# Optimization experiments

Hardware: AMD Instinct MI355X
Metric: run time of the kernel (lower is better)

## Reference

```python
import jax, jax.numpy as jnp
import numpy as np

B, N, D = 4, 4096, 128
R, K, O = 4, 16, 128


def setup_inputs() -> dict:
    key = jax.random.key(0)
    k1, k2, k3, k4 = jax.random.split(key, 4)
    node_features = jax.random.normal(k1, (B, N, D), dtype=jnp.float32)
    # index 0 selects the zero-pad row; valid node i is index i+1
    neighbor_indices = jax.random.randint(k2, (B, R, N, K), 0, N + 1, dtype=jnp.int32)
    relation_kernels = jax.random.normal(k3, (R, D, O), dtype=jnp.float32) * (1.0 / np.sqrt(D))
    self_kernel = jax.random.normal(k4, (D, O), dtype=jnp.float32) * (1.0 / np.sqrt(D))
    bias = jnp.zeros((O,), dtype=jnp.float32)
    return {
        "node_features": node_features,
        "neighbor_indices": neighbor_indices,
        "relation_kernels": relation_kernels,
        "self_kernel": self_kernel,
        "bias": bias,
    }


def reference(node_features, neighbor_indices, relation_kernels, self_kernel, bias):
    b, n, d = node_features.shape
    # prepend zero row so index 0 acts as padding (matches tf.concat zero_pad)
    padded = jnp.concatenate(
        [jnp.zeros((b, 1, d), node_features.dtype), node_features], axis=1
    )  # [B, N+1, D]
    # batched gather (tf.gather batch_dims=1): [B, R, N, K, D]
    neighbor_features = jax.vmap(lambda p, i: p[i])(padded, neighbor_indices)
    aggregated = neighbor_features.mean(axis=3)  # [B, R, N, D]
    # per-relation matmul then sum over relations
    total_msg = jnp.einsum("brnd,rdo->bno", aggregated, relation_kernels)
    self_msg = jnp.einsum("bnd,do->bno", node_features, self_kernel)
    out = total_msg + self_msg + bias
    return jax.nn.relu(out)  # dropout is identity at inference (rate=0.0)
```

## Files before the change

kernel.cpp:

```cpp
#include <hip/hip_runtime.h>
#include <cstddef>

namespace {
constexpr int B_ = 4, N_ = 4096, D_ = 128, R_ = 4, K_ = 16, O_ = 128;
constexpr int NP1 = N_ + 1;
constexpr int TN = 16;
constexpr int THREADS = 512;
constexpr int KK = (R_ + 1) * D_;
constexpr int PITCH_A = KK + 8;
}

typedef __bf16 bf16x8 __attribute__((ext_vector_type(8)));
typedef __bf16 bf16x4 __attribute__((ext_vector_type(4)));
typedef float  f32x4v __attribute__((ext_vector_type(4)));
typedef float  f32x2v __attribute__((ext_vector_type(2)));
using u32 = unsigned int;

__global__ __launch_bounds__(256)
void prep_all(const float* __restrict__ nf, const float* __restrict__ relk,
              const float* __restrict__ selfk,
              __bf16* __restrict__ ptab, unsigned char* __restrict__ ptab8,
              __bf16* __restrict__ wt) {
    int t = blockIdx.x * 256 + threadIdx.x;
    const int total_tab = B_ * NP1 * (D_ / 4);
    if (t < total_tab) {
        const int b   = t / (NP1 * 32);
        const int rem = t % (NP1 * 32);
        const int row = rem >> 5;
        const int q   = rem & 31;
        bf16x4 res;
        if (row == 0) {
            res[0] = (__bf16)0.f; res[1] = (__bf16)0.f;
            res[2] = (__bf16)0.f; res[3] = (__bf16)0.f;
        } else {
            const float4 v = *(const float4*)(nf + ((size_t)b * N_ + (row - 1)) * D_ + q * 4);
            res[0] = (__bf16)v.x; res[1] = (__bf16)v.y;
            res[2] = (__bf16)v.z; res[3] = (__bf16)v.w;
        }
        *(bf16x4*)(ptab + ((size_t)b * NP1 + row) * D_ + q * 4) = res;
        return;
    }
    t -= total_tab;
    if (t < total_tab) {
        const int b   = t / (NP1 * 32);
        const int rem = t % (NP1 * 32);
        const int row = rem >> 5;
        const int q   = rem & 31;
        u32 v8 = 0u;
        if (row != 0) {
            const float4 v = *(const float4*)(nf + ((size_t)b * N_ + (row - 1)) * D_ + q * 4);
            v8 = (u32)__builtin_amdgcn_cvt_pk_fp8_f32(v.x, v.y, 0, false);
            v8 = (u32)__builtin_amdgcn_cvt_pk_fp8_f32(v.z, v.w, (int)v8, true);
        }
        *(u32*)(ptab8 + ((size_t)b * NP1 + row) * D_ + q * 4) = v8;
        return;
    }
    t -= total_tab;
    if (t < O_ * (KK / 4)) {
        const int o   = t / (KK / 4);
        const int kk  = (t % (KK / 4)) * 4;
        bf16x4 res;
        #pragma unroll
        for (int i = 0; i < 4; ++i) {
            const int kki = kk + i;
            const float w = (kki < R_ * D_) ? relk[(size_t)kki * O_ + o]
                                            : selfk[(size_t)(kki - R_ * D_) * O_ + o];
            res[i] = (__bf16)w;
        }
        *(bf16x4*)(wt + (size_t)o * KK + kk) = res;
    }
}

__global__ __launch_bounds__(THREADS, 4)
void gcn_fused(const __bf16* __restrict__ ptab,
               const unsigned char* __restrict__ ptab8,
               const int*    __restrict__ nbr,
               const __bf16* __restrict__ wt,
               const float*  __restrict__ bias,
               float*        __restrict__ out)
{
    __shared__ __bf16 agg[TN][PITCH_A];

    const int hw   = blockIdx.x;
    const int xcd  = hw & 7;
    const int b    = xcd >> 1;
    const int tile = (xcd & 1) + ((hw >> 3) << 1);
    const int n0   = tile * TN;

    const int tid = threadIdx.x;
    const int wv  = tid >> 6;
    const int l   = tid & 63;

    {
        const int r    = wv & 3;
        const int nb   = (wv >> 2) * 8;
        const int nloc = l >> 3;
        const int cch  = l & 7;
        const int ioff = __builtin_amdgcn_readfirstlane(
            (((b * R_ + r) * N_) + n0 + nb) * K_);
        const int* __restrict__ ib = nbr + ioff;
        const unsigned char* __restrict__ tb8 = ptab8 + (size_t)b * NP1 * D_;

        f32x2v acc0 = {0.f,0.f}, acc1 = {0.f,0.f}, acc2 = {0.f,0.f}, acc3 = {0.f,0.f};
        f32x2v acc4 = {0.f,0.f}, acc5 = {0.f,0.f}, acc6 = {0.f,0.f}, acc7 = {0.f,0.f};

        #pragma unroll
        for (int k4 = 0; k4 < 4; ++k4) {
            const int4 iq = *(const int4*)(ib + nloc * K_ + k4 * 4);
            #define GCN_ROW(IDX)                                                   \
            {                                                                      \
                const uint4 u = *(const uint4*)(tb8 + (size_t)(IDX) * D_ + cch*16);\
                acc0 += __builtin_amdgcn_cvt_pk_f32_fp8(u.x, false);               \
                acc1 += __builtin_amdgcn_cvt_pk_f32_fp8(u.x, true);                \
                acc2 += __builtin_amdgcn_cvt_pk_f32_fp8(u.y, false);               \
                acc3 += __builtin_amdgcn_cvt_pk_f32_fp8(u.y, true);                \
                acc4 += __builtin_amdgcn_cvt_pk_f32_fp8(u.z, false);               \
                acc5 += __builtin_amdgcn_cvt_pk_f32_fp8(u.z, true);                \
                acc6 += __builtin_amdgcn_cvt_pk_f32_fp8(u.w, false);               \
                acc7 += __builtin_amdgcn_cvt_pk_f32_fp8(u.w, true);                \
            }
            GCN_ROW(iq.x) GCN_ROW(iq.y) GCN_ROW(iq.z) GCN_ROW(iq.w)
            #undef GCN_ROW
        }

        constexpr float s = 1.0f / (float)K_;
        bf16x8 r0, r1;
        r0[0] = (__bf16)(acc0.x * s); r0[1] = (__bf16)(acc0.y * s);
        r0[2] = (__bf16)(acc1.x * s); r0[3] = (__bf16)(acc1.y * s);
        r0[4] = (__bf16)(acc2.x * s); r0[5] = (__bf16)(acc2.y * s);
        r0[6] = (__bf16)(acc3.x * s); r0[7] = (__bf16)(acc3.y * s);
        r1[0] = (__bf16)(acc4.x * s); r1[1] = (__bf16)(acc4.y * s);
        r1[2] = (__bf16)(acc5.x * s); r1[3] = (__bf16)(acc5.y * s);
        r1[4] = (__bf16)(acc6.x * s); r1[5] = (__bf16)(acc6.y * s);
        r1[6] = (__bf16)(acc7.x * s); r1[7] = (__bf16)(acc7.y * s);
        __bf16* dst = &agg[nb + nloc][r * D_ + cch * 16];
        *(bf16x8*)(dst)     = r0;
        *(bf16x8*)(dst + 8) = r1;

        #pragma unroll
        for (int j = 0; j < 2; ++j) {
            const int n = wv * 2 + j;
            const u32 u = *((const u32*)(ptab + ((size_t)b * NP1 + n0 + n + 1) * D_) + l);
            *((u32*)&agg[n][R_ * D_] + l) = u;
        }
    }
    __syncthreads();

    const int lr = l & 15;
    const int lk = l >> 4;
    const int ct = wv;

    const __bf16* __restrict__ wr = wt + (size_t)(ct * 16 + lr) * KK + lk * 8;
    const __bf16* arow = &agg[lr][lk * 8];

    f32x4v acc = {0.f, 0.f, 0.f, 0.f};
    #pragma unroll 5
    for (int k0 = 0; k0 < KK; k0 += 32) {
        const bf16x8 a  = *(const bf16x8*)(arow + k0);
        const bf16x8 bf = *(const bf16x8*)(wr + k0);
        acc = __builtin_amdgcn_mfma_f32_16x16x32_bf16(a, bf, acc, 0, 0, 0);
    }

    const float bv = bias[ct * 16 + lr];
    #pragma unroll
    for (int j = 0; j < 4; ++j) {
        const int row = lk * 4 + j;
        out[((size_t)b * N_ + n0 + row) * O_ + ct * 16 + lr] = fmaxf(acc[j] + bv, 0.f);
    }
}

extern "C" void kernel_launch(void* const* d_in, const int* in_sizes, int n_in,
                              void* d_out, int out_size, void* d_ws, size_t ws_size,
                              hipStream_t stream) {
    const float* nf    = (const float*)d_in[0];
    const int*   nbr   = (const int*)  d_in[1];
    const float* relk  = (const float*)d_in[2];
    const float* selfk = (const float*)d_in[3];
    const float* bias  = (const float*)d_in[4];
    float* outp = (float*)d_out;

    __bf16* ptab = (__bf16*)d_ws;
    __bf16* wtp  = ptab + (size_t)B_ * NP1 * D_;
    unsigned char* ptab8 = (unsigned char*)(wtp + (size_t)O_ * KK);

    {
        const int total = 2 * B_ * NP1 * (D_ / 4) + O_ * (KK / 4);
        prep_all<<<(total + 255) / 256, 256, 0, stream>>>(nf, relk, selfk,
                                                          ptab, ptab8, wtp);
    }

    dim3 grid(B_ * (N_ / TN));
    gcn_fused<<<grid, THREADS, 0, stream>>>(ptab, ptab8, nbr, wtp, bias, outp);
}
```

Baseline: 37.17 us.

## Double node tile per block, reuse weight fragments across two MFMA row tiles

Raises the node tile from 16 to 32 per block so each weight fragment loaded from global memory feeds two MFMAs, halving weight traffic per output row and the number of blocks. The self-feature part of the GEMM now reads bf16 rows straight from global memory instead of staging them in shared memory, which shrinks the LDS tile. Each gather thread now handles two nodes with all index loads issued up front. The grid is halved (512 blocks), which lowers parallelism, and per-thread register pressure goes up.

```diff
diff --git a/kernel.cpp b/kernel.cpp
--- a/kernel.cpp
+++ b/kernel.cpp
@@ -4,10 +4,11 @@
 namespace {
 constexpr int B_ = 4, N_ = 4096, D_ = 128, R_ = 4, K_ = 16, O_ = 128;
 constexpr int NP1 = N_ + 1;
-constexpr int TN = 16;
+constexpr int TN = 32;
 constexpr int THREADS = 512;
 constexpr int KK = (R_ + 1) * D_;
-constexpr int PITCH_A = KK + 8;
+constexpr int KR = R_ * D_;
+constexpr int PITCH_A = KR + 8;
 }
 
 typedef __bf16 bf16x8 __attribute__((ext_vector_type(8)));
@@ -63,8 +64,8 @@
         #pragma unroll
         for (int i = 0; i < 4; ++i) {
             const int kki = kk + i;
-            const float w = (kki < R_ * D_) ? relk[(size_t)kki * O_ + o]
-                                            : selfk[(size_t)(kki - R_ * D_) * O_ + o];
+            const float w = (kki < KR) ? relk[(size_t)kki * O_ + o]
+                                       : selfk[(size_t)(kki - KR) * O_ + o];
             res[i] = (__bf16)w;
         }
         *(bf16x4*)(wt + (size_t)o * KK + kk) = res;
@@ -93,56 +94,73 @@
 
     {
         const int r    = wv & 3;
-        const int nb   = (wv >> 2) * 8;
+        const int ob   = (wv >> 2) * 8;
         const int nloc = l >> 3;
         const int cch  = l & 7;
         const int ioff = __builtin_amdgcn_readfirstlane(
-            (((b * R_ + r) * N_) + n0 + nb) * K_);
+            (((b * R_ + r) * N_) + n0) * K_);
         const int* __restrict__ ib = nbr + ioff;
         const unsigned char* __restrict__ tb8 = ptab8 + (size_t)b * NP1 * D_;
 
-        f32x2v acc0 = {0.f,0.f}, acc1 = {0.f,0.f}, acc2 = {0.f,0.f}, acc3 = {0.f,0.f};
-        f32x2v acc4 = {0.f,0.f}, acc5 = {0.f,0.f}, acc6 = {0.f,0.f}, acc7 = {0.f,0.f};
-
-        #pragma unroll
-        for (int k4 = 0; k4 < 4; ++k4) {
-            const int4 iq = *(const int4*)(ib + nloc * K_ + k4 * 4);
-            #define GCN_ROW(IDX)                                                   \
-            {                                                                      \
-                const uint4 u = *(const uint4*)(tb8 + (size_t)(IDX) * D_ + cch*16);\
-                acc0 += __builtin_amdgcn_cvt_pk_f32_fp8(u.x, false);               \
-                acc1 += __builtin_amdgcn_cvt_pk_f32_fp8(u.x, true);                \
-                acc2 += __builtin_amdgcn_cvt_pk_f32_fp8(u.y, false);               \
-                acc3 += __builtin_amdgcn_cvt_pk_f32_fp8(u.y, true);                \
-                acc4 += __builtin_amdgcn_cvt_pk_f32_fp8(u.z, false);               \
-                acc5 += __builtin_amdgcn_cvt_pk_f32_fp8(u.z, true);                \
-                acc6 += __builtin_amdgcn_cvt_pk_f32_fp8(u.w, false);               \
-                acc7 += __builtin_amdgcn_cvt_pk_f32_fp8(u.w, true);                \
-            }
-            GCN_ROW(iq.x) GCN_ROW(iq.y) GCN_ROW(iq.z) GCN_ROW(iq.w)
-            #undef GCN_ROW
-        }
-
+        const int na  = ob + nloc;
+        const int nb2 = na + 16;
+        const int4 ia0 = *(const int4*)(ib + na  * K_ + 0);
+        const int4 ia1 = *(const int4*)(ib + na  * K_ + 4);
+        const int4 ia2 = *(const int4*)(ib + na  * K_ + 8);
+        const int4 ia3 = *(const int4*)(ib + na  * K_ + 12);
+        const int4 ja0 = *(const int4*)(ib + nb2 * K_ + 0);
+        const int4 ja1 = *(const int4*)(ib + nb2 * K_ + 4);
+        const int4 ja2 = *(const int4*)(ib + nb2 * K_ + 8);
+        const int4 ja3 = *(const int4*)(ib + nb2 * K_ + 12);
+
+        f32x2v acc0, acc1, acc2, acc3, acc4, acc5, acc6, acc7;
         constexpr float s = 1.0f / (float)K_;
-        bf16x8 r0, r1;
-        r0[0] = (__bf16)(acc0.x * s); r0[1] = (__bf16)(acc0.y * s);
-        r0[2] = (__bf16)(acc1.x * s); r0[3] = (__bf16)(acc1.y * s);
-        r0[4] = (__bf16)(acc2.x * s); r0[5] = (__bf16)(acc2.y * s);
-        r0[6] = (__bf16)(acc3.x * s); r0[7] = (__bf16)(acc3.y * s);
-        r1[0] = (__bf16)(acc4.x * s); r1[1] = (__bf16)(acc4.y * s);
-        r1[2] = (__bf16)(acc5.x * s); r1[3] = (__bf16)(acc5.y * s);
-        r1[4] = (__bf16)(acc6.x * s); r1[5] = (__bf16)(acc6.y * s);
-        r1[6] = (__bf16)(acc7.x * s); r1[7] = (__bf16)(acc7.y * s);
-        __bf16* dst = &agg[nb + nloc][r * D_ + cch * 16];
-        *(bf16x8*)(dst)     = r0;
-        *(bf16x8*)(dst + 8) = r1;
-
-        #pragma unroll
-        for (int j = 0; j < 2; ++j) {
-            const int n = wv * 2 + j;
-            const u32 u = *((const u32*)(ptab + ((size_t)b * NP1 + n0 + n + 1) * D_) + l);
-            *((u32*)&agg[n][R_ * D_] + l) = u;
-        }
+
+        #define GCN_ROW(IDX)                                                   \
+        {                                                                      \
+            const uint4 u = *(const uint4*)(tb8 + (size_t)(IDX) * D_ + cch*16);\
+            acc0 += __builtin_amdgcn_cvt_pk_f32_fp8(u.x, false);               \
+            acc1 += __builtin_amdgcn_cvt_pk_f32_fp8(u.x, true);                \
+            acc2 += __builtin_amdgcn_cvt_pk_f32_fp8(u.y, false);               \
+            acc3 += __builtin_amdgcn_cvt_pk_f32_fp8(u.y, true);                \
+            acc4 += __builtin_amdgcn_cvt_pk_f32_fp8(u.z, false);               \
+            acc5 += __builtin_amdgcn_cvt_pk_f32_fp8(u.z, true);                \
+            acc6 += __builtin_amdgcn_cvt_pk_f32_fp8(u.w, false);               \
+            acc7 += __builtin_amdgcn_cvt_pk_f32_fp8(u.w, true);                \
+        }
+        #define GCN_PACK_STORE(ROW)                                            \
+        {                                                                      \
+            bf16x8 r0, r1;                                                     \
+            r0[0] = (__bf16)(acc0.x * s); r0[1] = (__bf16)(acc0.y * s);        \
+            r0[2] = (__bf16)(acc1.x * s); r0[3] = (__bf16)(acc1.y * s);        \
+            r0[4] = (__bf16)(acc2.x * s); r0[5] = (__bf16)(acc2.y * s);        \
+            r0[6] = (__bf16)(acc3.x * s); r0[7] = (__bf16)(acc3.y * s);        \
+            r1[0] = (__bf16)(acc4.x * s); r1[1] = (__bf16)(acc4.y * s);        \
+            r1[2] = (__bf16)(acc5.x * s); r1[3] = (__bf16)(acc5.y * s);        \
+            r1[4] = (__bf16)(acc6.x * s); r1[5] = (__bf16)(acc6.y * s);        \
+            r1[6] = (__bf16)(acc7.x * s); r1[7] = (__bf16)(acc7.y * s);        \
+            __bf16* dst = &agg[ROW][r * D_ + cch * 16];                        \
+            *(bf16x8*)(dst)     = r0;                                          \
+            *(bf16x8*)(dst + 8) = r1;                                          \
+        }
+
+        acc0 = {0.f,0.f}; acc1 = {0.f,0.f}; acc2 = {0.f,0.f}; acc3 = {0.f,0.f};
+        acc4 = {0.f,0.f}; acc5 = {0.f,0.f}; acc6 = {0.f,0.f}; acc7 = {0.f,0.f};
+        GCN_ROW(ia0.x) GCN_ROW(ia0.y) GCN_ROW(ia0.z) GCN_ROW(ia0.w)
+        GCN_ROW(ia1.x) GCN_ROW(ia1.y) GCN_ROW(ia1.z) GCN_ROW(ia1.w)
+        GCN_ROW(ia2.x) GCN_ROW(ia2.y) GCN_ROW(ia2.z) GCN_ROW(ia2.w)
+        GCN_ROW(ia3.x) GCN_ROW(ia3.y) GCN_ROW(ia3.z) GCN_ROW(ia3.w)
+        GCN_PACK_STORE(na)
+
+        acc0 = {0.f,0.f}; acc1 = {0.f,0.f}; acc2 = {0.f,0.f}; acc3 = {0.f,0.f};
+        acc4 = {0.f,0.f}; acc5 = {0.f,0.f}; acc6 = {0.f,0.f}; acc7 = {0.f,0.f};
+        GCN_ROW(ja0.x) GCN_ROW(ja0.y) GCN_ROW(ja0.z) GCN_ROW(ja0.w)
+        GCN_ROW(ja1.x) GCN_ROW(ja1.y) GCN_ROW(ja1.z) GCN_ROW(ja1.w)
+        GCN_ROW(ja2.x) GCN_ROW(ja2.y) GCN_ROW(ja2.z) GCN_ROW(ja2.w)
+        GCN_ROW(ja3.x) GCN_ROW(ja3.y) GCN_ROW(ja3.z) GCN_ROW(ja3.w)
+        GCN_PACK_STORE(nb2)
+        #undef GCN_ROW
+        #undef GCN_PACK_STORE
     }
     __syncthreads();
 
@@ -151,21 +169,40 @@
     const int ct = wv;
 
     const __bf16* __restrict__ wr = wt + (size_t)(ct * 16 + lr) * KK + lk * 8;
-    const __bf16* arow = &agg[lr][lk * 8];
-
-    f32x4v acc = {0.f, 0.f, 0.f, 0.f};
-    #pragma unroll 5
-    for (int k0 = 0; k0 < KK; k0 += 32) {
-        const bf16x8 a  = *(const bf16x8*)(arow + k0);
-        const bf16x8 bf = *(const bf16x8*)(wr + k0);
-        acc = __builtin_amdgcn_mfma_f32_16x16x32_bf16(a, bf, acc, 0, 0, 0);
+    const __bf16* a0p = &agg[lr][lk * 8];
+    const __bf16* a1p = &agg[lr + 16][lk * 8];
+
+    f32x4v acc0 = {0.f, 0.f, 0.f, 0.f};
+    f32x4v acc1 = {0.f, 0.f, 0.f, 0.f};
+    #pragma unroll 4
+    for (int k0 = 0; k0 < KR; k0 += 32) {
+        const bf16x8 w  = *(const bf16x8*)(wr + k0);
+        const bf16x8 a0 = *(const bf16x8*)(a0p + k0);
+        const bf16x8 a1 = *(const bf16x8*)(a1p + k0);
+        acc0 = __builtin_amdgcn_mfma_f32_16x16x32_bf16(a0, w, acc0, 0, 0, 0);
+        acc1 = __builtin_amdgcn_mfma_f32_16x16x32_bf16(a1, w, acc1, 0, 0, 0);
+    }
+    {
+        const __bf16* __restrict__ sp0 =
+            ptab + ((size_t)b * NP1 + n0 + lr + 1) * D_ + lk * 8;
+        const __bf16* __restrict__ sp1 = sp0 + 16 * D_;
+        #pragma unroll
+        for (int k0 = 0; k0 < D_; k0 += 32) {
+            const bf16x8 w  = *(const bf16x8*)(wr + KR + k0);
+            const bf16x8 a0 = *(const bf16x8*)(sp0 + k0);
+            const bf16x8 a1 = *(const bf16x8*)(sp1 + k0);
+            acc0 = __builtin_amdgcn_mfma_f32_16x16x32_bf16(a0, w, acc0, 0, 0, 0);
+            acc1 = __builtin_amdgcn_mfma_f32_16x16x32_bf16(a1, w, acc1, 0, 0, 0);
+        }
     }
 
     const float bv = bias[ct * 16 + lr];
     #pragma unroll
     for (int j = 0; j < 4; ++j) {
         const int row = lk * 4 + j;
-        out[((size_t)b * N_ + n0 + row) * O_ + ct * 16 + lr] = fmaxf(acc[j] + bv, 0.f);
+        float* op = out + ((size_t)b * N_ + n0 + row) * O_ + ct * 16 + lr;
+        op[0]        = fmaxf(acc0[j] + bv, 0.f);
+        op[16 * O_]  = fmaxf(acc1[j] + bv, 0.f);
     }
 }
 
```

Result: faster. 31.96 us (-14.0%).
